# Kernel optimization log

Measured on AMD Instinct MI355X. Metric: run time of the kernel, lower is better.

The kernel has to match this reference:

```python
import jax, jax.numpy as jnp
import numpy as np

NUM_TREES = 100
TREE_DEPTH = 5
INPUT_DIM = 256
NUM_CLASSES = 64
BATCH = 8192
NUM_NODES = 2 ** TREE_DEPTH - 1   # 31 decision nodes per tree
NUM_LEAVES = 2 ** TREE_DEPTH      # 32 leaves per tree


def setup_inputs() -> dict:
    key = jax.random.key(0)
    k_x, k_w, k_b, k_l = jax.random.split(key, 4)
    x = jax.random.normal(k_x, (BATCH, INPUT_DIM), dtype=jnp.float32)
    # stacked per-tree decision-node params (torch.randn init)
    node_w = jax.random.normal(k_w, (NUM_TREES, NUM_NODES, INPUT_DIM), dtype=jnp.float32)
    node_b = jax.random.normal(k_b, (NUM_TREES, NUM_NODES), dtype=jnp.float32)
    leaves = jax.random.normal(k_l, (NUM_TREES, NUM_LEAVES, NUM_CLASSES), dtype=jnp.float32)
    return {"x": x, "node_w": node_w, "node_b": node_b, "leaves": leaves}


def reference(x, node_w, node_b, leaves):
    # x: [B, D]; node_w: [T, Nn, D]; node_b: [T, Nn]; leaves: [T, Nl, C]
    T = node_w.shape[0]
    B = x.shape[0]
    depth = int(np.log2(leaves.shape[1]))
    idx = jnp.zeros((T, B), dtype=jnp.int32)
    for _ in range(depth):  # small fixed depth loop
        # gather each sample's routing node per tree: [T, B, D] and [T, B]
        w_g = jnp.take_along_axis(node_w, idx[:, :, None], axis=1)
        b_g = jnp.take_along_axis(node_b, idx, axis=1)
        decisions = jax.nn.sigmoid(jnp.einsum('tbd,bd->tb', w_g, x) + b_g)
        idx = 2 * idx + (decisions <= 0.5).astype(jnp.int32)
    # leaf gather: [T, B, C], then forest average over trees -> [B, C]
    tree_preds = jnp.take_along_axis(leaves, idx[:, :, None], axis=1)
    return jnp.mean(tree_preds, axis=0)
```

## Files before the change

### kernel.cpp

```cpp
#include <hip/hip_runtime.h>


typedef __bf16 bf16;
typedef __attribute__((ext_vector_type(8))) __bf16 bf16x8;
typedef __attribute__((ext_vector_type(4))) float f32x4;

#define NTREES 100
#define NB     8192
#define ND     256
#define NNODES 31
#define NLEAF  32
#define NCLS   64
#define TAU    2.0e-3f
#define QCAP   8192

__global__ void split_x_swz(const float* __restrict__ x,
                            bf16* __restrict__ xh, bf16* __restrict__ xl,
                            unsigned int* __restrict__ qcount) {
    if (blockIdx.x == 0 && threadIdx.x == 0) *qcount = 0;
    int i = blockIdx.x * 256 + threadIdx.x;
    int m  = i & 15;
    int dq = (i >> 4) & 31;
    int g  = i >> 9;
    const float* src = x + (size_t)(g * 16 + m) * ND + dq * 8;
    bf16x8 h8, l8;
#pragma unroll
    for (int e = 0; e < 8; ++e) {
        float f = src[e];
        bf16 h = (bf16)f;
        h8[e] = h;
        l8[e] = (bf16)(f - (float)h);
    }
    *(bf16x8*)(xh + (size_t)i * 8) = h8;
    *(bf16x8*)(xl + (size_t)i * 8) = l8;
}

__global__ __launch_bounds__(256, 3) void forest_fused(
    const bf16* __restrict__ xh, const bf16* __restrict__ xl,
    const float* __restrict__ wf,
    const float* __restrict__ bias,
    unsigned char* __restrict__ idxb,
    unsigned int* __restrict__ qcount, unsigned int* __restrict__ queue)
{
    __shared__ char lds[50176];
    bf16*  Wh  = (bf16*)lds;
    bf16*  Wl  = (bf16*)(lds + 16384);
    float* scr = (float*)(lds + 32768);

    const int tid  = threadIdx.x;
    const int wave = tid >> 6;
    const int lane = tid & 63;
    const int m    = lane & 15;
    const int q    = lane >> 4;
    const int tg   = blockIdx.x;
    const int mg   = blockIdx.y;
    const int gbase = mg * 16 + wave * 4;

    float biasv[4];
#pragma unroll
    for (int ni = 0; ni < 4; ++ni)
        biasv[ni] = bias[(size_t)(tg * 4 + ni) * NNODES + m];

    f32x4 acc[4][4];
#pragma unroll
    for (int mi = 0; mi < 4; ++mi)
#pragma unroll
        for (int ni = 0; ni < 4; ++ni)
            acc[mi][ni] = (f32x4){0.f, 0.f, 0.f, 0.f};

    const int srow = wave * 16 + (lane & 15);
    const float* wrow = wf + ((size_t)(tg * 4 + (srow >> 4)) * NNODES + (srow & 15)) * ND;

#pragma unroll
    for (int kc = 0; kc < 2; ++kc) {
        __syncthreads();
#pragma unroll
        for (int it = 0; it < 4; ++it) {
            int c = (lane >> 4) + it * 4;
            const float* src = wrow + kc * 128 + c * 8;
            float4 f0 = *(const float4*)(src);
            float4 f1 = *(const float4*)(src + 4);
            float fv[8] = {f0.x, f0.y, f0.z, f0.w, f1.x, f1.y, f1.z, f1.w};
            bf16x8 h8, l8;
#pragma unroll
            for (int e = 0; e < 8; ++e) {
                bf16 h = (bf16)fv[e];
                h8[e] = h;
                l8[e] = (bf16)(fv[e] - (float)h);
            }
            int swz = c ^ (srow & 7);
            *(bf16x8*)(Wh + srow * 128 + swz * 8) = h8;
            *(bf16x8*)(Wl + srow * 128 + swz * 8) = l8;
        }
        __syncthreads();

        bf16x8 cah[4], cal[4], nah[4], nal[4];
#pragma unroll
        for (int mi = 0; mi < 4; ++mi) {
            size_t off = (size_t)(gbase + mi) * 4096 + (size_t)(kc * 16) * 128 + lane * 8;
            cah[mi] = *(const bf16x8*)(xh + off);
            cal[mi] = *(const bf16x8*)(xl + off);
        }
#pragma unroll
        for (int kk = 0; kk < 4; ++kk) {
            if (kk < 3) {
#pragma unroll
                for (int mi = 0; mi < 4; ++mi) {
                    size_t off = (size_t)(gbase + mi) * 4096
                               + (size_t)(kc * 16 + (kk + 1) * 4) * 128 + lane * 8;
                    nah[mi] = *(const bf16x8*)(xh + off);
                    nal[mi] = *(const bf16x8*)(xl + off);
                }
            }
#pragma unroll
            for (int ni = 0; ni < 4; ++ni) {
                const int n    = ni * 16 + m;
                const int cidx = (4 * kk + q) ^ (m & 7);
                bf16x8 bh = *(const bf16x8*)(Wh + n * 128 + cidx * 8);
                bf16x8 bl = *(const bf16x8*)(Wl + n * 128 + cidx * 8);
#pragma unroll
                for (int mi = 0; mi < 4; ++mi) {
                    acc[mi][ni] = __builtin_amdgcn_mfma_f32_16x16x32_bf16(cal[mi], bh, acc[mi][ni], 0, 0, 0);
                    acc[mi][ni] = __builtin_amdgcn_mfma_f32_16x16x32_bf16(cah[mi], bl, acc[mi][ni], 0, 0, 0);
                    acc[mi][ni] = __builtin_amdgcn_mfma_f32_16x16x32_bf16(cah[mi], bh, acc[mi][ni], 0, 0, 0);
                }
            }
#pragma unroll
            for (int mi = 0; mi < 4; ++mi) { cah[mi] = nah[mi]; cal[mi] = nal[mi]; }
        }
    }

    float* ws_ = scr + wave * (64 * 17);
    const int sg = mg * 256 + wave * 64 + lane;
    unsigned int pk = 0;
#pragma unroll
    for (int ni = 0; ni < 4; ++ni) {
#pragma unroll
        for (int mi = 0; mi < 4; ++mi)
#pragma unroll
            for (int r = 0; r < 4; ++r)
                ws_[(mi * 16 + q * 4 + r) * 17 + m] = acc[mi][ni][r] + biasv[ni];
        __syncthreads();
        int node = 0;
        float mn = 1e30f;
#pragma unroll
        for (int lvl = 0; lvl < 5; ++lvl) {
            float z = ws_[lane * 17 + node];
            mn = fminf(mn, fabsf(z));
            node = 2 * node + (z <= 0.0f ? 1 : 0);
        }
        pk |= (unsigned)node << (8 * ni);
        if (mn < TAU) {
            unsigned int pos = atomicAdd(qcount, 1u);
            if (pos < QCAP)
                queue[pos] = ((unsigned)(tg * 4 + ni) << 13) | (unsigned)sg;
        }
        __syncthreads();
    }
    *(unsigned int*)(idxb + (size_t)sg * NTREES + tg * 4) = pk;
}

__global__ void fixup_kernel(const float* __restrict__ x, const float* __restrict__ wf,
                             const float* __restrict__ bias,
                             const unsigned int* __restrict__ qcount,
                             const unsigned int* __restrict__ queue,
                             unsigned char* __restrict__ idxb) {
    const int wid  = (blockIdx.x * 256 + threadIdx.x) >> 6;
    const int lane = threadIdx.x & 63;
    unsigned int n = *qcount;
    if (n > QCAP) n = QCAP;
    for (unsigned int it = wid; it < n; it += 256) {
        unsigned int e = queue[it];
        int t = e >> 13, s = e & 8191;
        const float* xr = x + (size_t)s * ND;
        float4 xv = *(const float4*)(xr + lane * 4);
        int node = 0;
        for (int lvl = 0; lvl < 5; ++lvl) {
            const float* wr = wf + ((size_t)t * NNODES + node) * ND;
            float4 wv = *(const float4*)(wr + lane * 4);
            double zz = (double)xv.x * wv.x + (double)xv.y * wv.y
                      + (double)xv.z * wv.z + (double)xv.w * wv.w;
#pragma unroll
            for (int o = 32; o > 0; o >>= 1) zz += __shfl_xor(zz, o);
            zz += (double)bias[t * NNODES + node];
            node = 2 * node + (zz <= 0.0 ? 1 : 0);
        }
        if (lane == 0) idxb[(size_t)s * NTREES + t] = (unsigned char)node;
    }
}

__global__ void leaf_gather(const unsigned char* __restrict__ idxb,
                            const float* __restrict__ leaves,
                            float* __restrict__ out) {
    const int wave = threadIdx.x >> 6;
    const int lane = threadIdx.x & 63;
    const int s = blockIdx.x * 4 + wave;
    unsigned int rw = 0;
    if (lane < 25) rw = *(const unsigned int*)(idxb + (size_t)s * NTREES + lane * 4);
    float acc = 0.f;
#pragma unroll 10
    for (int t = 0; t < NTREES; ++t) {
        unsigned int wrd = __shfl(rw, t >> 2);
        int li = (wrd >> ((t & 3) * 8)) & 255;
        acc += leaves[((size_t)t * NLEAF + li) * NCLS + lane];
    }
    out[(size_t)s * NCLS + lane] = acc * 0.01f;
}

extern "C" void kernel_launch(void* const* d_in, const int* in_sizes, int n_in,
                              void* d_out, int out_size, void* d_ws, size_t ws_size,
                              hipStream_t stream) {
    const float* x  = (const float*)d_in[0];
    const float* nw = (const float*)d_in[1];
    const float* nb = (const float*)d_in[2];
    const float* lv = (const float*)d_in[3];
    float* out = (float*)d_out;

    char* ws = (char*)d_ws;
    bf16* xh = (bf16*)(ws + 0);
    bf16* xl = (bf16*)(ws + 4194304);
    unsigned char* idxb  = (unsigned char*)(ws + 8388608);
    unsigned int* qcount = (unsigned int*)(ws + 9207808);
    unsigned int* queue  = (unsigned int*)(ws + 9207824);
    if (ws_size < (size_t)9240592) return;

    split_x_swz<<<NB * ND / (256 * 8), 256, 0, stream>>>(x, xh, xl, qcount);
    forest_fused<<<dim3(NTREES / 4, NB / 256), 256, 0, stream>>>(
        xh, xl, nw, nb, idxb, qcount, queue);
    fixup_kernel<<<64, 256, 0, stream>>>(x, nw, nb, qcount, queue, idxb);
    leaf_gather<<<NB / 4, 256, 0, stream>>>(idxb, lv, out);
}
```

Baseline: 118.5 us.

## Fuse x bf16 split and near-threshold fixup into the main forest kernel

Removes the separate x-splitting kernel and the global fixup kernel. The main kernel now loads fp32 x directly, splits it into hi/lo bf16 in registers, and recomputes near-threshold decisions in fp64 through a per-block LDS queue before writing leaf indices. This saves two launches and the 4 MB round trip of split x through global memory. In exchange, every tree-group block repeats the split arithmetic and reads fp32 x, which is twice the bytes of the bf16 copies. The per-block queue is capped at 32 entries, so overflow items would silently keep the approximate decision.

```diff
diff --git a/kernel.cpp b/kernel.cpp
--- a/kernel.cpp
+++ b/kernel.cpp
@@ -12,40 +12,21 @@
 #define NLEAF  32
 #define NCLS   64
 #define TAU    2.0e-3f
-#define QCAP   8192
-
-__global__ void split_x_swz(const float* __restrict__ x,
-                            bf16* __restrict__ xh, bf16* __restrict__ xl,
-                            unsigned int* __restrict__ qcount) {
-    if (blockIdx.x == 0 && threadIdx.x == 0) *qcount = 0;
-    int i = blockIdx.x * 256 + threadIdx.x;
-    int m  = i & 15;
-    int dq = (i >> 4) & 31;
-    int g  = i >> 9;
-    const float* src = x + (size_t)(g * 16 + m) * ND + dq * 8;
-    bf16x8 h8, l8;
-#pragma unroll
-    for (int e = 0; e < 8; ++e) {
-        float f = src[e];
-        bf16 h = (bf16)f;
-        h8[e] = h;
-        l8[e] = (bf16)(f - (float)h);
-    }
-    *(bf16x8*)(xh + (size_t)i * 8) = h8;
-    *(bf16x8*)(xl + (size_t)i * 8) = l8;
-}
-
-__global__ __launch_bounds__(256, 3) void forest_fused(
-    const bf16* __restrict__ xh, const bf16* __restrict__ xl,
+#define FQCAP  32
+
+__global__ __launch_bounds__(256, 3) void forest_all(
+    const float* __restrict__ x,
     const float* __restrict__ wf,
     const float* __restrict__ bias,
-    unsigned char* __restrict__ idxb,
-    unsigned int* __restrict__ qcount, unsigned int* __restrict__ queue)
+    unsigned char* __restrict__ idxb)
 {
     __shared__ char lds[50176];
     bf16*  Wh  = (bf16*)lds;
     bf16*  Wl  = (bf16*)(lds + 16384);
     float* scr = (float*)(lds + 32768);
+    __shared__ int fcnt;
+    __shared__ unsigned short fitems[FQCAP];
+    __shared__ unsigned char  fres[FQCAP];
 
     const int tid  = threadIdx.x;
     const int wave = tid >> 6;
@@ -54,7 +35,8 @@
     const int q    = lane >> 4;
     const int tg   = blockIdx.x;
     const int mg   = blockIdx.y;
-    const int gbase = mg * 16 + wave * 4;
+
+    if (tid == 0) fcnt = 0;
 
     float biasv[4];
 #pragma unroll
@@ -67,6 +49,11 @@
 #pragma unroll
         for (int ni = 0; ni < 4; ++ni)
             acc[mi][ni] = (f32x4){0.f, 0.f, 0.f, 0.f};
+
+    const float* xbase[4];
+#pragma unroll
+    for (int mi = 0; mi < 4; ++mi)
+        xbase[mi] = x + (size_t)(mg * 256 + wave * 64 + mi * 16 + m) * ND + q * 8;
 
     const int srow = wave * 16 + (lane & 15);
     const float* wrow = wf + ((size_t)(tg * 4 + (srow >> 4)) * NNODES + (srow & 15)) * ND;
@@ -94,22 +81,33 @@
         }
         __syncthreads();
 
-        bf16x8 cah[4], cal[4], nah[4], nal[4];
+        float4 ca[4], cb[4], na[4], nb2[4];
 #pragma unroll
         for (int mi = 0; mi < 4; ++mi) {
-            size_t off = (size_t)(gbase + mi) * 4096 + (size_t)(kc * 16) * 128 + lane * 8;
-            cah[mi] = *(const bf16x8*)(xh + off);
-            cal[mi] = *(const bf16x8*)(xl + off);
+            const float* p = xbase[mi] + kc * 128;
+            ca[mi] = *(const float4*)p;
+            cb[mi] = *(const float4*)(p + 4);
         }
 #pragma unroll
         for (int kk = 0; kk < 4; ++kk) {
             if (kk < 3) {
 #pragma unroll
                 for (int mi = 0; mi < 4; ++mi) {
-                    size_t off = (size_t)(gbase + mi) * 4096
-                               + (size_t)(kc * 16 + (kk + 1) * 4) * 128 + lane * 8;
-                    nah[mi] = *(const bf16x8*)(xh + off);
-                    nal[mi] = *(const bf16x8*)(xl + off);
+                    const float* p = xbase[mi] + kc * 128 + (kk + 1) * 32;
+                    na[mi]  = *(const float4*)p;
+                    nb2[mi] = *(const float4*)(p + 4);
+                }
+            }
+            bf16x8 ah[4], al[4];
+#pragma unroll
+            for (int mi = 0; mi < 4; ++mi) {
+                float fv[8] = {ca[mi].x, ca[mi].y, ca[mi].z, ca[mi].w,
+                               cb[mi].x, cb[mi].y, cb[mi].z, cb[mi].w};
+#pragma unroll
+                for (int e = 0; e < 8; ++e) {
+                    bf16 h = (bf16)fv[e];
+                    ah[mi][e] = h;
+                    al[mi][e] = (bf16)(fv[e] - (float)h);
                 }
             }
 #pragma unroll
@@ -120,18 +118,19 @@
                 bf16x8 bl = *(const bf16x8*)(Wl + n * 128 + cidx * 8);
 #pragma unroll
                 for (int mi = 0; mi < 4; ++mi) {
-                    acc[mi][ni] = __builtin_amdgcn_mfma_f32_16x16x32_bf16(cal[mi], bh, acc[mi][ni], 0, 0, 0);
-                    acc[mi][ni] = __builtin_amdgcn_mfma_f32_16x16x32_bf16(cah[mi], bl, acc[mi][ni], 0, 0, 0);
-                    acc[mi][ni] = __builtin_amdgcn_mfma_f32_16x16x32_bf16(cah[mi], bh, acc[mi][ni], 0, 0, 0);
+                    acc[mi][ni] = __builtin_amdgcn_mfma_f32_16x16x32_bf16(al[mi], bh, acc[mi][ni], 0, 0, 0);
+                    acc[mi][ni] = __builtin_amdgcn_mfma_f32_16x16x32_bf16(ah[mi], bl, acc[mi][ni], 0, 0, 0);
+                    acc[mi][ni] = __builtin_amdgcn_mfma_f32_16x16x32_bf16(ah[mi], bh, acc[mi][ni], 0, 0, 0);
                 }
             }
 #pragma unroll
-            for (int mi = 0; mi < 4; ++mi) { cah[mi] = nah[mi]; cal[mi] = nal[mi]; }
+            for (int mi = 0; mi < 4; ++mi) { ca[mi] = na[mi]; cb[mi] = nb2[mi]; }
         }
     }
 
     float* ws_ = scr + wave * (64 * 17);
-    const int sg = mg * 256 + wave * 64 + lane;
+    const int s_l = wave * 64 + lane;
+    const int sg  = mg * 256 + s_l;
     unsigned int pk = 0;
 #pragma unroll
     for (int ni = 0; ni < 4; ++ni) {
@@ -151,28 +150,19 @@
         }
         pk |= (unsigned)node << (8 * ni);
         if (mn < TAU) {
-            unsigned int pos = atomicAdd(qcount, 1u);
-            if (pos < QCAP)
-                queue[pos] = ((unsigned)(tg * 4 + ni) << 13) | (unsigned)sg;
-        }
-        __syncthreads();
-    }
-    *(unsigned int*)(idxb + (size_t)sg * NTREES + tg * 4) = pk;
-}
-
-__global__ void fixup_kernel(const float* __restrict__ x, const float* __restrict__ wf,
-                             const float* __restrict__ bias,
-                             const unsigned int* __restrict__ qcount,
-                             const unsigned int* __restrict__ queue,
-                             unsigned char* __restrict__ idxb) {
-    const int wid  = (blockIdx.x * 256 + threadIdx.x) >> 6;
-    const int lane = threadIdx.x & 63;
-    unsigned int n = *qcount;
-    if (n > QCAP) n = QCAP;
-    for (unsigned int it = wid; it < n; it += 256) {
-        unsigned int e = queue[it];
-        int t = e >> 13, s = e & 8191;
-        const float* xr = x + (size_t)s * ND;
+            int p = atomicAdd(&fcnt, 1);
+            if (p < FQCAP) fitems[p] = (unsigned short)((s_l << 2) | ni);
+        }
+        __syncthreads();
+    }
+
+    int cnt = fcnt;
+    if (cnt > FQCAP) cnt = FQCAP;
+    for (int i = wave; i < cnt; i += 4) {
+        int it  = fitems[i];
+        int sl2 = it >> 2, ni = it & 3;
+        int t   = tg * 4 + ni;
+        const float* xr = x + (size_t)(mg * 256 + sl2) * ND;
         float4 xv = *(const float4*)(xr + lane * 4);
         int node = 0;
         for (int lvl = 0; lvl < 5; ++lvl) {
@@ -185,8 +175,18 @@
             zz += (double)bias[t * NNODES + node];
             node = 2 * node + (zz <= 0.0 ? 1 : 0);
         }
-        if (lane == 0) idxb[(size_t)s * NTREES + t] = (unsigned char)node;
-    }
+        if (lane == 0) fres[i] = (unsigned char)node;
+    }
+    __syncthreads();
+
+    for (int i = 0; i < cnt; ++i) {
+        int it = fitems[i];
+        if ((it >> 2) == s_l) {
+            int ni = it & 3;
+            pk = (pk & ~(255u << (8 * ni))) | ((unsigned)fres[i] << (8 * ni));
+        }
+    }
+    *(unsigned int*)(idxb + (size_t)sg * NTREES + tg * 4) = pk;
 }
 
 __global__ void leaf_gather(const unsigned char* __restrict__ idxb,
@@ -216,17 +216,9 @@
     const float* lv = (const float*)d_in[3];
     float* out = (float*)d_out;
 
-    char* ws = (char*)d_ws;
-    bf16* xh = (bf16*)(ws + 0);
-    bf16* xl = (bf16*)(ws + 4194304);
-    unsigned char* idxb  = (unsigned char*)(ws + 8388608);
-    unsigned int* qcount = (unsigned int*)(ws + 9207808);
-    unsigned int* queue  = (unsigned int*)(ws + 9207824);
-    if (ws_size < (size_t)9240592) return;
-
-    split_x_swz<<<NB * ND / (256 * 8), 256, 0, stream>>>(x, xh, xl, qcount);
-    forest_fused<<<dim3(NTREES / 4, NB / 256), 256, 0, stream>>>(
-        xh, xl, nw, nb, idxb, qcount, queue);
-    fixup_kernel<<<64, 256, 0, stream>>>(x, nw, nb, qcount, queue, idxb);
+    unsigned char* idxb = (unsigned char*)d_ws;
+    if (ws_size < (size_t)819200) return;
+
+    forest_all<<<dim3(NTREES / 4, NB / 256), 256, 0, stream>>>(x, nw, nb, idxb);
     leaf_gather<<<NB / 4, 256, 0, stream>>>(idxb, lv, out);
 }
```

After: 119.2 us. About the same (+0.6%).
